# Optimization experiments

Measured on AMD Instinct MI355X. Metric: run time of the kernel, lower is better.

## Reference

```python
import jax, jax.numpy as jnp
import numpy as np

N_NODES = 100000
N_EDGES = 600000
VOCAB = 50000
EMBED_DIM = 128
HIDDEN_DIM = 128


def gcn_conv(h, W, b, src, dst, n_nodes):
    """PyG GCNConv: x' = D^{-1/2} (A+I) D^{-1/2} X W + b.
    src/dst already include self-loops."""
    hw = h @ W                                   # [N, out]
    deg = jnp.zeros((n_nodes,), hw.dtype).at[dst].add(1.0)   # in-degree incl. self-loop
    dinv = jax.lax.rsqrt(deg)                    # deg >= 1 thanks to self-loops
    norm = dinv[src] * dinv[dst]                 # [E+N]
    msgs = norm[:, None] * hw[src]               # gather [E+N, out]
    out = jnp.zeros_like(hw).at[dst].add(msgs)   # scatter-aggregate
    return out + b


def setup_inputs() -> dict:
    key = jax.random.key(0)
    ks = jax.random.split(key, 8)
    x = jax.random.randint(ks[0], (N_NODES,), 0, VOCAB, dtype=jnp.int64 if jax.config.jax_enable_x64 else jnp.int32)
    edge_index = jax.random.randint(ks[1], (2, N_EDGES), 0, N_NODES, dtype=jnp.int32)
    emb = jax.random.normal(ks[2], (VOCAB, EMBED_DIM), dtype=jnp.float32)
    # Glorot-style scale for GCN weights
    W1 = jax.random.normal(ks[3], (EMBED_DIM, HIDDEN_DIM), dtype=jnp.float32) * (1.0 / np.sqrt(EMBED_DIM))
    b1 = jnp.zeros((HIDDEN_DIM,), dtype=jnp.float32)
    W2 = jax.random.normal(ks[4], (HIDDEN_DIM, HIDDEN_DIM), dtype=jnp.float32) * (1.0 / np.sqrt(HIDDEN_DIM))
    b2 = jnp.zeros((HIDDEN_DIM,), dtype=jnp.float32)
    return {"x": x, "edge_index": edge_index, "emb": emb, "W1": W1, "b1": b1, "W2": W2, "b2": b2}


def reference(x, edge_index, emb, W1, b1, W2, b2):
    n = x.shape[0]
    loops = jnp.arange(n, dtype=edge_index.dtype)
    src = jnp.concatenate([edge_index[0], loops])  # add self-loops once
    dst = jnp.concatenate([edge_index[1], loops])
    h = emb[x]                                     # [N, embed_dim] embedding lookup
    h = jax.nn.relu(gcn_conv(h, W1, b1, src, dst, n))
    h = jax.nn.relu(gcn_conv(h, W2, b2, src, dst, n))
    return h
```

## Files before the change

### kernel.cpp

```cpp
#include <hip/hip_runtime.h>
#include <hip/hip_fp16.h>


#define NDIM 128
#define PAD_K 136
#define SCAN_IPT 4
#define SCAN_BLK 256
#define SCAN_IPB (SCAN_BLK * SCAN_IPT)

typedef __bf16 bf16x8 __attribute__((ext_vector_type(8)));
typedef float f32x4 __attribute__((ext_vector_type(4)));

__device__ __forceinline__ float bf2f(unsigned short u) {
    union { unsigned int i; float f; } c;
    c.i = (unsigned int)u << 16;
    return c.f;
}
__device__ __forceinline__ unsigned short f2bf(float f) {
    __bf16 b = (__bf16)f;
    return __builtin_bit_cast(unsigned short, b);
}
__device__ __forceinline__ unsigned short f2h(float f) {
    __half h = __float2half_rn(f);
    return __builtin_bit_cast(unsigned short, h);
}
__device__ __forceinline__ float h2f(unsigned short u) {
    return __half2float(__builtin_bit_cast(__half, u));
}
__device__ __forceinline__ void unpack8(uint4 q, float* f) {
    f[0] = bf2f((unsigned short)(q.x & 0xffff));
    f[1] = bf2f((unsigned short)(q.x >> 16));
    f[2] = bf2f((unsigned short)(q.y & 0xffff));
    f[3] = bf2f((unsigned short)(q.y >> 16));
    f[4] = bf2f((unsigned short)(q.z & 0xffff));
    f[5] = bf2f((unsigned short)(q.z >> 16));
    f[6] = bf2f((unsigned short)(q.w & 0xffff));
    f[7] = bf2f((unsigned short)(q.w >> 16));
}

__global__ void degree_count(const int* __restrict__ dst, int* __restrict__ cnt, int E) {
    const int stride = gridDim.x * blockDim.x;
    int e = blockIdx.x * blockDim.x + threadIdx.x;
#pragma unroll
    for (int k = 0; k < 2; ++k) {
        int ee = e + k * stride;
        if (ee < E) atomicAdd(&cnt[dst[ee]], 1);
    }
}

__global__ void scan_blocks(const int* __restrict__ in, int* __restrict__ out,
                            int* __restrict__ bsums, int n) {
    __shared__ int lds[SCAN_BLK];
    const int t = threadIdx.x;
    const int base = blockIdx.x * SCAN_IPB + t * SCAN_IPT;
    int v[SCAN_IPT];
    int s = 0;
#pragma unroll
    for (int k = 0; k < SCAN_IPT; ++k) { v[k] = (base + k < n) ? in[base + k] : 0; s += v[k]; }
    lds[t] = s;
    __syncthreads();
    for (int off = 1; off < SCAN_BLK; off <<= 1) {
        int x = (t >= off) ? lds[t - off] : 0;
        __syncthreads();
        lds[t] += x;
        __syncthreads();
    }
    if (t == SCAN_BLK - 1) bsums[blockIdx.x] = lds[t];
    int run = (t == 0) ? 0 : lds[t - 1];
#pragma unroll
    for (int k = 0; k < SCAN_IPT; ++k) {
        if (base + k < n) out[base + k] = run;
        run += v[k];
    }
}

__global__ void scan_partials(int* __restrict__ bsums, int nb) {
    __shared__ int lds[128];
    const int t = threadIdx.x;
    lds[t] = (t < nb) ? bsums[t] : 0;
    __syncthreads();
    for (int off = 1; off < 128; off <<= 1) {
        int x = (t >= off) ? lds[t - off] : 0;
        __syncthreads();
        lds[t] += x;
        __syncthreads();
    }
    if (t < nb) bsums[t] = (t == 0) ? 0 : lds[t - 1];
}

__global__ void add_offsets_dinv_wt(int* __restrict__ rp, const int* __restrict__ bsums,
                                    const int* __restrict__ cnt, float* __restrict__ dinv, int n,
                                    int nblkA,
                                    const float* __restrict__ W1, const float* __restrict__ W2,
                                    unsigned short* __restrict__ WT1,
                                    unsigned short* __restrict__ WT2) {
    if ((int)blockIdx.x < nblkA) {
        int i = blockIdx.x * blockDim.x + threadIdx.x;
        if (i < n) {
            rp[i] += bsums[i / SCAN_IPB];
            dinv[i] = rsqrtf((float)cnt[i] + 1.0f);
        }
    } else {
        int c = (blockIdx.x - nblkA) * blockDim.x + threadIdx.x;
        int cc = c & 16383;
        int j = cc >> 7, k = cc & 127;
        if (c < 16384) WT1[cc] = f2bf(W1[k * 128 + j]);
        else if (c < 32768) WT2[cc] = f2bf(W2[k * 128 + j]);
    }
}

__global__ __launch_bounds__(256, 4)
void gemm1_fill(const float* __restrict__ emb, const unsigned short* __restrict__ WT1,
                unsigned short* __restrict__ embW1, int V, int gemmBlocks,
                const int* __restrict__ src, const int* __restrict__ dst,
                int* __restrict__ rp, const int* __restrict__ x,
                const float* __restrict__ dinv, int2* __restrict__ ew, int E,
                int fillBlocks) {
    __shared__ __bf16 sBT[128 * PAD_K];
    const int tid = threadIdx.x;

    if ((int)blockIdx.x < gemmBlocks) {
        const int rbase = blockIdx.x * 64;
        {
            const uint4* bsrc = (const uint4*)WT1;
#pragma unroll
            for (int i = 0; i < 8; ++i) {
                int c = tid + i * 256;
                int j = c >> 4, u = c & 15;
                *(uint4*)&sBT[j * PAD_K + u * 8] = bsrc[c];
            }
        }
        __syncthreads();

        const int wave = tid >> 6, lane = tid & 63;
        const int quad = lane >> 4, lrow = lane & 15;
        int arow = rbase + wave * 16 + lrow;
        if (arow >= V) arow = V - 1;

        f32x4 acc[8];
#pragma unroll
        for (int nt = 0; nt < 8; ++nt) acc[nt] = (f32x4)0.0f;

#pragma unroll
        for (int ks = 0; ks < 4; ++ks) {
            const int kb = ks * 32 + quad * 8;
            const float4* A4 = (const float4*)emb;
            float4 v0 = A4[(size_t)arow * 32 + (kb >> 2)];
            float4 v1 = A4[(size_t)arow * 32 + (kb >> 2) + 1];
            bf16x8 a = (bf16x8){(__bf16)v0.x, (__bf16)v0.y, (__bf16)v0.z, (__bf16)v0.w,
                                (__bf16)v1.x, (__bf16)v1.y, (__bf16)v1.z, (__bf16)v1.w};
#pragma unroll
            for (int nt = 0; nt < 8; ++nt) {
                bf16x8 b = *(const bf16x8*)&sBT[(nt * 16 + lrow) * PAD_K + kb];
                acc[nt] = __builtin_amdgcn_mfma_f32_16x16x32_bf16(a, b, acc[nt], 0, 0, 0);
            }
        }

#pragma unroll
        for (int r = 0; r < 4; ++r) {
            int grow = rbase + wave * 16 + quad * 4 + r;
            if (grow < V) {
                unsigned short* orow = embW1 + (size_t)grow * NDIM + lrow;
#pragma unroll
                for (int nt = 0; nt < 8; ++nt)
                    orow[nt * 16] = f2bf(acc[nt][r]);
            }
        }
    } else {
        const int bid = blockIdx.x - gemmBlocks;
        const int stride = fillBlocks * 256;
        int e = bid * 256 + tid;
#pragma unroll
        for (int k = 0; k < 2; ++k, e += stride) {
            if (e < E) {
                int d = dst[e], s = src[e];
                int xs = x[s];
                float ds = dinv[s];
                int p = atomicAdd(&rp[d], 1);
                ew[p] = make_int2(s, (int)(((unsigned)f2h(ds) << 16) | (unsigned)xs));
            }
        }
    }
}

__global__ __launch_bounds__(256, 4)
void gemm_mfma_b(const unsigned short* __restrict__ Asrc, const unsigned short* __restrict__ WTb,
                 const float* __restrict__ dinv, unsigned short* __restrict__ outb, int n) {
    __shared__ __bf16 sBT[128 * PAD_K];
    const int tid = threadIdx.x;
    const int rbase = blockIdx.x * 64;

    {
        const uint4* bsrc = (const uint4*)WTb;
#pragma unroll
        for (int i = 0; i < 8; ++i) {
            int c = tid + i * 256;
            int j = c >> 4, u = c & 15;
            *(uint4*)&sBT[j * PAD_K + u * 8] = bsrc[c];
        }
    }
    __syncthreads();

    const int wave = tid >> 6, lane = tid & 63;
    const int quad = lane >> 4, lrow = lane & 15;
    int arow = rbase + wave * 16 + lrow;
    if (arow >= n) arow = n - 1;

    f32x4 acc[8];
#pragma unroll
    for (int nt = 0; nt < 8; ++nt) acc[nt] = (f32x4)0.0f;

#pragma unroll
    for (int ks = 0; ks < 4; ++ks) {
        const int kb = ks * 32 + quad * 8;
        bf16x8 a = *(const bf16x8*)(Asrc + (size_t)arow * 128 + kb);
#pragma unroll
        for (int nt = 0; nt < 8; ++nt) {
            bf16x8 b = *(const bf16x8*)&sBT[(nt * 16 + lrow) * PAD_K + kb];
            acc[nt] = __builtin_amdgcn_mfma_f32_16x16x32_bf16(a, b, acc[nt], 0, 0, 0);
        }
    }

#pragma unroll
    for (int r = 0; r < 4; ++r) {
        int grow = rbase + wave * 16 + quad * 4 + r;
        if (grow < n) {
            float dsc = dinv[grow];
            unsigned short* orow = outb + (size_t)grow * NDIM + lrow;
#pragma unroll
            for (int nt = 0; nt < 8; ++nt)
                orow[nt * 16] = f2bf(dsc * acc[nt][r]);
        }
    }
}

__global__ void aggregate1(const unsigned short* __restrict__ tab, const int* __restrict__ x,
                           const int* __restrict__ rp, const int2* __restrict__ ew,
                           const float* __restrict__ dinv, const float* __restrict__ bias,
                           unsigned short* __restrict__ outb, int n, int half) {
    int t = blockIdx.x * blockDim.x + threadIdx.x;
    int g = t >> 4, u = t & 15;
    if (g >= half) return;
    const uint4* tab4 = (const uint4*)tab;
    const int i0 = g, i1 = g + half;
    const bool has1 = (i1 < n);
    float di0 = dinv[i0];
    float di1 = has1 ? dinv[i1] : 0.0f;
    float acc0[8], acc1[8];
    {
        float f[8];
        unpack8(tab4[(size_t)x[i0] * 16 + u], f);
#pragma unroll
        for (int k = 0; k < 8; ++k) acc0[k] = di0 * f[k];
    }
    if (has1) {
        float f[8];
        unpack8(tab4[(size_t)x[i1] * 16 + u], f);
#pragma unroll
        for (int k = 0; k < 8; ++k) acc1[k] = di1 * f[k];
    }
    int j0 = (i0 == 0) ? 0 : rp[i0 - 1];
    const int e0 = rp[i0];
    int j1 = has1 ? rp[i1 - 1] : 0;
    const int e1 = has1 ? rp[i1] : 0;

    while (j0 + 2 <= e0 && j1 + 2 <= e1) {
        int2 a0 = ew[j0], a1 = ew[j0 + 1], c0 = ew[j1], c1 = ew[j1 + 1];
        uint4 qa0 = tab4[(size_t)(a0.y & 0xffff) * 16 + u];
        uint4 qa1 = tab4[(size_t)(a1.y & 0xffff) * 16 + u];
        uint4 qc0 = tab4[(size_t)(c0.y & 0xffff) * 16 + u];
        uint4 qc1 = tab4[(size_t)(c1.y & 0xffff) * 16 + u];
        float fa0[8], fa1[8], fc0[8], fc1[8];
        unpack8(qa0, fa0); unpack8(qa1, fa1); unpack8(qc0, fc0); unpack8(qc1, fc1);
        float na0 = h2f((unsigned short)((unsigned)a0.y >> 16));
        float na1 = h2f((unsigned short)((unsigned)a1.y >> 16));
        float nc0 = h2f((unsigned short)((unsigned)c0.y >> 16));
        float nc1 = h2f((unsigned short)((unsigned)c1.y >> 16));
#pragma unroll
        for (int k = 0; k < 8; ++k) {
            acc0[k] += fmaf(na0, fa0[k], na1 * fa1[k]);
            acc1[k] += fmaf(nc0, fc0[k], nc1 * fc1[k]);
        }
        j0 += 2; j1 += 2;
    }
    for (; j0 + 2 <= e0; j0 += 2) {
        int2 a0 = ew[j0], a1 = ew[j0 + 1];
        uint4 qa0 = tab4[(size_t)(a0.y & 0xffff) * 16 + u];
        uint4 qa1 = tab4[(size_t)(a1.y & 0xffff) * 16 + u];
        float fa0[8], fa1[8];
        unpack8(qa0, fa0); unpack8(qa1, fa1);
        float na0 = h2f((unsigned short)((unsigned)a0.y >> 16));
        float na1 = h2f((unsigned short)((unsigned)a1.y >> 16));
#pragma unroll
        for (int k = 0; k < 8; ++k) acc0[k] += fmaf(na0, fa0[k], na1 * fa1[k]);
    }
    if (j0 < e0) {
        int2 a = ew[j0];
        uint4 q = tab4[(size_t)(a.y & 0xffff) * 16 + u];
        float f[8];
        unpack8(q, f);
        float nm = h2f((unsigned short)((unsigned)a.y >> 16));
#pragma unroll
        for (int k = 0; k < 8; ++k) acc0[k] = fmaf(nm, f[k], acc0[k]);
    }
    for (; j1 + 2 <= e1; j1 += 2) {
        int2 c0 = ew[j1], c1 = ew[j1 + 1];
        uint4 qc0 = tab4[(size_t)(c0.y & 0xffff) * 16 + u];
        uint4 qc1 = tab4[(size_t)(c1.y & 0xffff) * 16 + u];
        float fc0[8], fc1[8];
        unpack8(qc0, fc0); unpack8(qc1, fc1);
        float nc0 = h2f((unsigned short)((unsigned)c0.y >> 16));
        float nc1 = h2f((unsigned short)((unsigned)c1.y >> 16));
#pragma unroll
        for (int k = 0; k < 8; ++k) acc1[k] += fmaf(nc0, fc0[k], nc1 * fc1[k]);
    }
    if (j1 < e1) {
        int2 c = ew[j1];
        uint4 q = tab4[(size_t)(c.y & 0xffff) * 16 + u];
        float f[8];
        unpack8(q, f);
        float nm = h2f((unsigned short)((unsigned)c.y >> 16));
#pragma unroll
        for (int k = 0; k < 8; ++k) acc1[k] = fmaf(nm, f[k], acc1[k]);
    }

    const float4 b0 = ((const float4*)bias)[u * 2];
    const float4 b1 = ((const float4*)bias)[u * 2 + 1];
    {
        float r[8];
        r[0] = fmaxf(fmaf(di0, acc0[0], b0.x), 0.0f);
        r[1] = fmaxf(fmaf(di0, acc0[1], b0.y), 0.0f);
        r[2] = fmaxf(fmaf(di0, acc0[2], b0.z), 0.0f);
        r[3] = fmaxf(fmaf(di0, acc0[3], b0.w), 0.0f);
        r[4] = fmaxf(fmaf(di0, acc0[4], b1.x), 0.0f);
        r[5] = fmaxf(fmaf(di0, acc0[5], b1.y), 0.0f);
        r[6] = fmaxf(fmaf(di0, acc0[6], b1.z), 0.0f);
        r[7] = fmaxf(fmaf(di0, acc0[7], b1.w), 0.0f);
        uint4 o;
        o.x = (unsigned)f2bf(r[0]) | ((unsigned)f2bf(r[1]) << 16);
        o.y = (unsigned)f2bf(r[2]) | ((unsigned)f2bf(r[3]) << 16);
        o.z = (unsigned)f2bf(r[4]) | ((unsigned)f2bf(r[5]) << 16);
        o.w = (unsigned)f2bf(r[6]) | ((unsigned)f2bf(r[7]) << 16);
        ((uint4*)outb)[(size_t)i0 * 16 + u] = o;
    }
    if (has1) {
        float r[8];
        r[0] = fmaxf(fmaf(di1, acc1[0], b0.x), 0.0f);
        r[1] = fmaxf(fmaf(di1, acc1[1], b0.y), 0.0f);
        r[2] = fmaxf(fmaf(di1, acc1[2], b0.z), 0.0f);
        r[3] = fmaxf(fmaf(di1, acc1[3], b0.w), 0.0f);
        r[4] = fmaxf(fmaf(di1, acc1[4], b1.x), 0.0f);
        r[5] = fmaxf(fmaf(di1, acc1[5], b1.y), 0.0f);
        r[6] = fmaxf(fmaf(di1, acc1[6], b1.z), 0.0f);
        r[7] = fmaxf(fmaf(di1, acc1[7], b1.w), 0.0f);
        uint4 o;
        o.x = (unsigned)f2bf(r[0]) | ((unsigned)f2bf(r[1]) << 16);
        o.y = (unsigned)f2bf(r[2]) | ((unsigned)f2bf(r[3]) << 16);
        o.z = (unsigned)f2bf(r[4]) | ((unsigned)f2bf(r[5]) << 16);
        o.w = (unsigned)f2bf(r[6]) | ((unsigned)f2bf(r[7]) << 16);
        ((uint4*)outb)[(size_t)i1 * 16 + u] = o;
    }
}

__global__ void aggregate2(const unsigned short* __restrict__ vs, const int* __restrict__ rp,
                           const int2* __restrict__ ew, const float* __restrict__ dinv,
                           const float* __restrict__ bias, float* __restrict__ out,
                           int n, int half) {
    int t = blockIdx.x * blockDim.x + threadIdx.x;
    int g = t >> 4, u = t & 15;
    if (g >= half) return;
    const uint4* vs4 = (const uint4*)vs;
    const int i0 = g, i1 = g + half;
    const bool has1 = (i1 < n);
    float acc0[8], acc1[8];
    unpack8(vs4[(size_t)i0 * 16 + u], acc0);
    if (has1) unpack8(vs4[(size_t)i1 * 16 + u], acc1);
    int j0 = (i0 == 0) ? 0 : rp[i0 - 1];
    const int e0 = rp[i0];
    int j1 = has1 ? rp[i1 - 1] : 0;
    const int e1 = has1 ? rp[i1] : 0;

    while (j0 + 2 <= e0 && j1 + 2 <= e1) {
        int s00 = ew[j0].x, s01 = ew[j0 + 1].x, s10 = ew[j1].x, s11 = ew[j1 + 1].x;
        uint4 q00 = vs4[(size_t)s00 * 16 + u];
        uint4 q01 = vs4[(size_t)s01 * 16 + u];
        uint4 q10 = vs4[(size_t)s10 * 16 + u];
        uint4 q11 = vs4[(size_t)s11 * 16 + u];
        float f00[8], f01[8], f10[8], f11[8];
        unpack8(q00, f00); unpack8(q01, f01); unpack8(q10, f10); unpack8(q11, f11);
#pragma unroll
        for (int k = 0; k < 8; ++k) {
            acc0[k] += f00[k] + f01[k];
            acc1[k] += f10[k] + f11[k];
        }
        j0 += 2; j1 += 2;
    }
    for (; j0 + 2 <= e0; j0 += 2) {
        int s00 = ew[j0].x, s01 = ew[j0 + 1].x;
        uint4 q00 = vs4[(size_t)s00 * 16 + u];
        uint4 q01 = vs4[(size_t)s01 * 16 + u];
        float f00[8], f01[8];
        unpack8(q00, f00); unpack8(q01, f01);
#pragma unroll
        for (int k = 0; k < 8; ++k) acc0[k] += f00[k] + f01[k];
    }
    if (j0 < e0) {
        uint4 q = vs4[(size_t)ew[j0].x * 16 + u];
        float f[8];
        unpack8(q, f);
#pragma unroll
        for (int k = 0; k < 8; ++k) acc0[k] += f[k];
    }
    for (; j1 + 2 <= e1; j1 += 2) {
        int s10 = ew[j1].x, s11 = ew[j1 + 1].x;
        uint4 q10 = vs4[(size_t)s10 * 16 + u];
        uint4 q11 = vs4[(size_t)s11 * 16 + u];
        float f10[8], f11[8];
        unpack8(q10, f10); unpack8(q11, f11);
#pragma unroll
        for (int k = 0; k < 8; ++k) acc1[k] += f10[k] + f11[k];
    }
    if (j1 < e1) {
        uint4 q = vs4[(size_t)ew[j1].x * 16 + u];
        float f[8];
        unpack8(q, f);
#pragma unroll
        for (int k = 0; k < 8; ++k) acc1[k] += f[k];
    }

    const float4 b0 = ((const float4*)bias)[u * 2];
    const float4 b1 = ((const float4*)bias)[u * 2 + 1];
    {
        float di = dinv[i0];
        float4 r0, r1;
        r0.x = fmaxf(fmaf(di, acc0[0], b0.x), 0.0f);
        r0.y = fmaxf(fmaf(di, acc0[1], b0.y), 0.0f);
        r0.z = fmaxf(fmaf(di, acc0[2], b0.z), 0.0f);
        r0.w = fmaxf(fmaf(di, acc0[3], b0.w), 0.0f);
        r1.x = fmaxf(fmaf(di, acc0[4], b1.x), 0.0f);
        r1.y = fmaxf(fmaf(di, acc0[5], b1.y), 0.0f);
        r1.z = fmaxf(fmaf(di, acc0[6], b1.z), 0.0f);
        r1.w = fmaxf(fmaf(di, acc0[7], b1.w), 0.0f);
        ((float4*)out)[(size_t)i0 * 32 + u * 2] = r0;
        ((float4*)out)[(size_t)i0 * 32 + u * 2 + 1] = r1;
    }
    if (has1) {
        float di = dinv[i1];
        float4 r0, r1;
        r0.x = fmaxf(fmaf(di, acc1[0], b0.x), 0.0f);
        r0.y = fmaxf(fmaf(di, acc1[1], b0.y), 0.0f);
        r0.z = fmaxf(fmaf(di, acc1[2], b0.z), 0.0f);
        r0.w = fmaxf(fmaf(di, acc1[3], b0.w), 0.0f);
        r1.x = fmaxf(fmaf(di, acc1[4], b1.x), 0.0f);
        r1.y = fmaxf(fmaf(di, acc1[5], b1.y), 0.0f);
        r1.z = fmaxf(fmaf(di, acc1[6], b1.z), 0.0f);
        r1.w = fmaxf(fmaf(di, acc1[7], b1.w), 0.0f);
        ((float4*)out)[(size_t)i1 * 32 + u * 2] = r0;
        ((float4*)out)[(size_t)i1 * 32 + u * 2 + 1] = r1;
    }
}

extern "C" void kernel_launch(void* const* d_in, const int* in_sizes, int n_in,
                              void* d_out, int out_size, void* d_ws, size_t ws_size,
                              hipStream_t stream) {
    const int* x = (const int*)d_in[0];
    const int* edge_index = (const int*)d_in[1];
    const float* emb = (const float*)d_in[2];
    const float* W1 = (const float*)d_in[3];
    const float* b1 = (const float*)d_in[4];
    const float* W2 = (const float*)d_in[5];
    const float* b2 = (const float*)d_in[6];
    float* out = (float*)d_out;

    const int N = in_sizes[0];
    const int E = in_sizes[1] / 2;
    const int V = in_sizes[2] / NDIM;
    const int* src = edge_index;
    const int* dst = edge_index + E;

    char* p = (char*)d_ws;
    auto alloc = [&](size_t bytes) {
        char* q = p;
        p += (bytes + 511) & ~(size_t)511;
        return q;
    };
    int* cnt = (int*)alloc((size_t)N * sizeof(int));
    int* rp = (int*)alloc((size_t)N * sizeof(int));
    float* dinv = (float*)alloc((size_t)N * sizeof(float));
    int* bsums = (int*)alloc(128 * sizeof(int));
    int2* ew = (int2*)alloc((size_t)E * sizeof(int2));
    unsigned short* WT1 = (unsigned short*)alloc(16384 * sizeof(unsigned short));
    unsigned short* WT2 = (unsigned short*)alloc(16384 * sizeof(unsigned short));
    unsigned short* embW1 = (unsigned short*)alloc((size_t)V * NDIM * sizeof(unsigned short));
    unsigned short* h1b = (unsigned short*)alloc((size_t)N * NDIM * sizeof(unsigned short));
    unsigned short* vs2 = (unsigned short*)alloc((size_t)N * NDIM * sizeof(unsigned short));
    (void)ws_size;

    const int NB = (N + SCAN_IPB - 1) / SCAN_IPB;
    const int nblkA = (N + 255) / 256;
    const int half = (N + 1) / 2;
    const int gemmBlocks = (V + 63) / 64;
    const int fillBlocks = (E / 2 + 255) / 256;

    hipMemsetAsync(cnt, 0, (size_t)N * sizeof(int), stream);
    degree_count<<<(E / 2 + 255) / 256, 256, 0, stream>>>(dst, cnt, E);
    scan_blocks<<<NB, SCAN_BLK, 0, stream>>>(cnt, rp, bsums, N);
    scan_partials<<<1, 128, 0, stream>>>(bsums, NB);
    add_offsets_dinv_wt<<<nblkA + 128, 256, 0, stream>>>(rp, bsums, cnt, dinv, N, nblkA,
                                                         W1, W2, WT1, WT2);

    gemm1_fill<<<gemmBlocks + fillBlocks, 256, 0, stream>>>(
        emb, WT1, embW1, V, gemmBlocks, src, dst, rp, x, dinv, ew, E, fillBlocks);

    const int agg_blocks = (int)(((size_t)half * 16 + 255) / 256);

    aggregate1<<<agg_blocks, 256, 0, stream>>>(embW1, x, rp, ew, dinv, b1, h1b, N, half);
    gemm_mfma_b<<<(N + 63) / 64, 256, 0, stream>>>(h1b, WT2, dinv, vs2, N);
    aggregate2<<<agg_blocks, 256, 0, stream>>>(vs2, rp, ew, dinv, b2, out, N, half);
}
```

Measured before the change: 242.1 us.

## Restructure CSR build: single-block scan fused into GEMM1, separate edge fill

Replaces the multi-kernel degree count, block scan, partial scan and offset-add sequence with three launches. The first counts degrees and transposes the weights. The second has block 0 scan the degree counts serially while the other blocks run the embedding GEMM. The third fills the edge list. This cuts kernel launches and grid-wide dependencies, and hides the scan behind the GEMM work. The cost is that the scan now runs in a single block over about 100k entries in roughly 98 sequential chunks, which may become the critical path. The edge fill also no longer overlaps with the GEMM.

```diff
diff --git a/kernel.cpp b/kernel.cpp
--- a/kernel.cpp
+++ b/kernel.cpp
@@ -4,9 +4,6 @@
 
 #define NDIM 128
 #define PAD_K 136
-#define SCAN_IPT 4
-#define SCAN_BLK 256
-#define SCAN_IPB (SCAN_BLK * SCAN_IPT)
 
 typedef __bf16 bf16x8 __attribute__((ext_vector_type(8)));
 typedef float f32x4 __attribute__((ext_vector_type(4)));
@@ -38,149 +35,121 @@
     f[7] = bf2f((unsigned short)(q.w >> 16));
 }
 
-__global__ void degree_count(const int* __restrict__ dst, int* __restrict__ cnt, int E) {
-    const int stride = gridDim.x * blockDim.x;
-    int e = blockIdx.x * blockDim.x + threadIdx.x;
-#pragma unroll
-    for (int k = 0; k < 2; ++k) {
-        int ee = e + k * stride;
-        if (ee < E) atomicAdd(&cnt[dst[ee]], 1);
-    }
-}
-
-__global__ void scan_blocks(const int* __restrict__ in, int* __restrict__ out,
-                            int* __restrict__ bsums, int n) {
-    __shared__ int lds[SCAN_BLK];
-    const int t = threadIdx.x;
-    const int base = blockIdx.x * SCAN_IPB + t * SCAN_IPT;
-    int v[SCAN_IPT];
-    int s = 0;
-#pragma unroll
-    for (int k = 0; k < SCAN_IPT; ++k) { v[k] = (base + k < n) ? in[base + k] : 0; s += v[k]; }
-    lds[t] = s;
-    __syncthreads();
-    for (int off = 1; off < SCAN_BLK; off <<= 1) {
-        int x = (t >= off) ? lds[t - off] : 0;
-        __syncthreads();
-        lds[t] += x;
-        __syncthreads();
-    }
-    if (t == SCAN_BLK - 1) bsums[blockIdx.x] = lds[t];
-    int run = (t == 0) ? 0 : lds[t - 1];
-#pragma unroll
-    for (int k = 0; k < SCAN_IPT; ++k) {
-        if (base + k < n) out[base + k] = run;
-        run += v[k];
-    }
-}
-
-__global__ void scan_partials(int* __restrict__ bsums, int nb) {
-    __shared__ int lds[128];
-    const int t = threadIdx.x;
-    lds[t] = (t < nb) ? bsums[t] : 0;
-    __syncthreads();
-    for (int off = 1; off < 128; off <<= 1) {
-        int x = (t >= off) ? lds[t - off] : 0;
-        __syncthreads();
-        lds[t] += x;
-        __syncthreads();
-    }
-    if (t < nb) bsums[t] = (t == 0) ? 0 : lds[t - 1];
-}
-
-__global__ void add_offsets_dinv_wt(int* __restrict__ rp, const int* __restrict__ bsums,
-                                    const int* __restrict__ cnt, float* __restrict__ dinv, int n,
-                                    int nblkA,
-                                    const float* __restrict__ W1, const float* __restrict__ W2,
-                                    unsigned short* __restrict__ WT1,
-                                    unsigned short* __restrict__ WT2) {
-    if ((int)blockIdx.x < nblkA) {
-        int i = blockIdx.x * blockDim.x + threadIdx.x;
-        if (i < n) {
-            rp[i] += bsums[i / SCAN_IPB];
-            dinv[i] = rsqrtf((float)cnt[i] + 1.0f);
-        }
-    } else {
-        int c = (blockIdx.x - nblkA) * blockDim.x + threadIdx.x;
+__global__ void count_wt(const int* __restrict__ dst, int* __restrict__ cnt, int E, int nWT,
+                         const float* __restrict__ W1, const float* __restrict__ W2,
+                         unsigned short* __restrict__ WT1, unsigned short* __restrict__ WT2) {
+    if ((int)blockIdx.x < nWT) {
+        int c = blockIdx.x * blockDim.x + threadIdx.x;
         int cc = c & 16383;
         int j = cc >> 7, k = cc & 127;
         if (c < 16384) WT1[cc] = f2bf(W1[k * 128 + j]);
         else if (c < 32768) WT2[cc] = f2bf(W2[k * 128 + j]);
+    } else {
+        int e = (blockIdx.x - nWT) * blockDim.x + threadIdx.x;
+        if (e < E) atomicAdd(&cnt[dst[e]], 1);
     }
 }
 
 __global__ __launch_bounds__(256, 4)
-void gemm1_fill(const float* __restrict__ emb, const unsigned short* __restrict__ WT1,
-                unsigned short* __restrict__ embW1, int V, int gemmBlocks,
-                const int* __restrict__ src, const int* __restrict__ dst,
-                int* __restrict__ rp, const int* __restrict__ x,
-                const float* __restrict__ dinv, int2* __restrict__ ew, int E,
-                int fillBlocks) {
+void scan_gemm1(const int* __restrict__ cnt, int* __restrict__ rp, float* __restrict__ dinv,
+                int n, const float* __restrict__ emb, const unsigned short* __restrict__ WT1,
+                unsigned short* __restrict__ embW1, int V) {
     __shared__ __bf16 sBT[128 * PAD_K];
     const int tid = threadIdx.x;
 
-    if ((int)blockIdx.x < gemmBlocks) {
-        const int rbase = blockIdx.x * 64;
-        {
-            const uint4* bsrc = (const uint4*)WT1;
-#pragma unroll
-            for (int i = 0; i < 8; ++i) {
-                int c = tid + i * 256;
-                int j = c >> 4, u = c & 15;
-                *(uint4*)&sBT[j * PAD_K + u * 8] = bsrc[c];
+    if (blockIdx.x == 0) {
+        int* lds = (int*)sBT;
+        int carry = 0;
+        for (int base = 0; base < n; base += 1024) {
+            const int idx = base + tid * 4;
+            int v[4];
+            int s = 0;
+#pragma unroll
+            for (int k = 0; k < 4; ++k) {
+                v[k] = (idx + k < n) ? cnt[idx + k] : 0;
+                s += v[k];
             }
-        }
-        __syncthreads();
-
-        const int wave = tid >> 6, lane = tid & 63;
-        const int quad = lane >> 4, lrow = lane & 15;
-        int arow = rbase + wave * 16 + lrow;
-        if (arow >= V) arow = V - 1;
-
-        f32x4 acc[8];
-#pragma unroll
-        for (int nt = 0; nt < 8; ++nt) acc[nt] = (f32x4)0.0f;
-
-#pragma unroll
-        for (int ks = 0; ks < 4; ++ks) {
-            const int kb = ks * 32 + quad * 8;
-            const float4* A4 = (const float4*)emb;
-            float4 v0 = A4[(size_t)arow * 32 + (kb >> 2)];
-            float4 v1 = A4[(size_t)arow * 32 + (kb >> 2) + 1];
-            bf16x8 a = (bf16x8){(__bf16)v0.x, (__bf16)v0.y, (__bf16)v0.z, (__bf16)v0.w,
-                                (__bf16)v1.x, (__bf16)v1.y, (__bf16)v1.z, (__bf16)v1.w};
-#pragma unroll
-            for (int nt = 0; nt < 8; ++nt) {
-                bf16x8 b = *(const bf16x8*)&sBT[(nt * 16 + lrow) * PAD_K + kb];
-                acc[nt] = __builtin_amdgcn_mfma_f32_16x16x32_bf16(a, b, acc[nt], 0, 0, 0);
+#pragma unroll
+            for (int k = 0; k < 4; ++k)
+                if (idx + k < n) dinv[idx + k] = rsqrtf((float)v[k] + 1.0f);
+            lds[tid] = s;
+            __syncthreads();
+            for (int off = 1; off < 256; off <<= 1) {
+                int x = (tid >= off) ? lds[tid - off] : 0;
+                __syncthreads();
+                lds[tid] += x;
+                __syncthreads();
             }
-        }
-
-#pragma unroll
-        for (int r = 0; r < 4; ++r) {
-            int grow = rbase + wave * 16 + quad * 4 + r;
-            if (grow < V) {
-                unsigned short* orow = embW1 + (size_t)grow * NDIM + lrow;
-#pragma unroll
-                for (int nt = 0; nt < 8; ++nt)
-                    orow[nt * 16] = f2bf(acc[nt][r]);
+            int run = carry + ((tid == 0) ? 0 : lds[tid - 1]);
+#pragma unroll
+            for (int k = 0; k < 4; ++k) {
+                if (idx + k < n) rp[idx + k] = run;
+                run += v[k];
             }
-        }
-    } else {
-        const int bid = blockIdx.x - gemmBlocks;
-        const int stride = fillBlocks * 256;
-        int e = bid * 256 + tid;
-#pragma unroll
-        for (int k = 0; k < 2; ++k, e += stride) {
-            if (e < E) {
-                int d = dst[e], s = src[e];
-                int xs = x[s];
-                float ds = dinv[s];
-                int p = atomicAdd(&rp[d], 1);
-                ew[p] = make_int2(s, (int)(((unsigned)f2h(ds) << 16) | (unsigned)xs));
-            }
-        }
-    }
+            carry += lds[255];
+            __syncthreads();
+        }
+        return;
+    }
+
+    const int rbase = (blockIdx.x - 1) * 64;
+    {
+        const uint4* bsrc = (const uint4*)WT1;
+#pragma unroll
+        for (int i = 0; i < 8; ++i) {
+            int c = tid + i * 256;
+            int j = c >> 4, u = c & 15;
+            *(uint4*)&sBT[j * PAD_K + u * 8] = bsrc[c];
+        }
+    }
+    __syncthreads();
+
+    const int wave = tid >> 6, lane = tid & 63;
+    const int quad = lane >> 4, lrow = lane & 15;
+    int arow = rbase + wave * 16 + lrow;
+    if (arow >= V) arow = V - 1;
+
+    f32x4 acc[8];
+#pragma unroll
+    for (int nt = 0; nt < 8; ++nt) acc[nt] = (f32x4)0.0f;
+
+#pragma unroll
+    for (int ks = 0; ks < 4; ++ks) {
+        const int kb = ks * 32 + quad * 8;
+        const float4* A4 = (const float4*)emb;
+        float4 v0 = A4[(size_t)arow * 32 + (kb >> 2)];
+        float4 v1 = A4[(size_t)arow * 32 + (kb >> 2) + 1];
+        bf16x8 a = (bf16x8){(__bf16)v0.x, (__bf16)v0.y, (__bf16)v0.z, (__bf16)v0.w,
+                            (__bf16)v1.x, (__bf16)v1.y, (__bf16)v1.z, (__bf16)v1.w};
+#pragma unroll
+        for (int nt = 0; nt < 8; ++nt) {
+            bf16x8 b = *(const bf16x8*)&sBT[(nt * 16 + lrow) * PAD_K + kb];
+            acc[nt] = __builtin_amdgcn_mfma_f32_16x16x32_bf16(a, b, acc[nt], 0, 0, 0);
+        }
+    }
+
+#pragma unroll
+    for (int r = 0; r < 4; ++r) {
+        int grow = rbase + wave * 16 + quad * 4 + r;
+        if (grow < V) {
+            unsigned short* orow = embW1 + (size_t)grow * NDIM + lrow;
+#pragma unroll
+            for (int nt = 0; nt < 8; ++nt)
+                orow[nt * 16] = f2bf(acc[nt][r]);
+        }
+    }
+}
+
+__global__ void fill_edges(const int* __restrict__ src, const int* __restrict__ dst,
+                           int* __restrict__ rp, const int* __restrict__ x,
+                           const float* __restrict__ dinv, int2* __restrict__ ew, int E) {
+    int e = blockIdx.x * blockDim.x + threadIdx.x;
+    if (e >= E) return;
+    int d = dst[e], s = src[e];
+    int xs = x[s];
+    float ds = dinv[s];
+    int p = atomicAdd(&rp[d], 1);
+    ew[p] = make_int2(s, (int)(((unsigned)f2h(ds) << 16) | (unsigned)xs));
 }
 
 __global__ __launch_bounds__(256, 4)
@@ -487,7 +456,6 @@
     int* cnt = (int*)alloc((size_t)N * sizeof(int));
     int* rp = (int*)alloc((size_t)N * sizeof(int));
     float* dinv = (float*)alloc((size_t)N * sizeof(float));
-    int* bsums = (int*)alloc(128 * sizeof(int));
     int2* ew = (int2*)alloc((size_t)E * sizeof(int2));
     unsigned short* WT1 = (unsigned short*)alloc(16384 * sizeof(unsigned short));
     unsigned short* WT2 = (unsigned short*)alloc(16384 * sizeof(unsigned short));
@@ -496,21 +464,15 @@
     unsigned short* vs2 = (unsigned short*)alloc((size_t)N * NDIM * sizeof(unsigned short));
     (void)ws_size;
 
-    const int NB = (N + SCAN_IPB - 1) / SCAN_IPB;
-    const int nblkA = (N + 255) / 256;
     const int half = (N + 1) / 2;
-    const int gemmBlocks = (V + 63) / 64;
-    const int fillBlocks = (E / 2 + 255) / 256;
+    const int nWT = 128;
+    const int cntBlocks = (E + 255) / 256;
+    const int gemm1Blocks = (V + 63) / 64;
 
     hipMemsetAsync(cnt, 0, (size_t)N * sizeof(int), stream);
-    degree_count<<<(E / 2 + 255) / 256, 256, 0, stream>>>(dst, cnt, E);
-    scan_blocks<<<NB, SCAN_BLK, 0, stream>>>(cnt, rp, bsums, N);
-    scan_partials<<<1, 128, 0, stream>>>(bsums, NB);
-    add_offsets_dinv_wt<<<nblkA + 128, 256, 0, stream>>>(rp, bsums, cnt, dinv, N, nblkA,
-                                                         W1, W2, WT1, WT2);
-
-    gemm1_fill<<<gemmBlocks + fillBlocks, 256, 0, stream>>>(
-        emb, WT1, embW1, V, gemmBlocks, src, dst, rp, x, dinv, ew, E, fillBlocks);
+    count_wt<<<nWT + cntBlocks, 256, 0, stream>>>(dst, cnt, E, nWT, W1, W2, WT1, WT2);
+    scan_gemm1<<<1 + gemm1Blocks, 256, 0, stream>>>(cnt, rp, dinv, N, emb, WT1, embW1, V);
+    fill_edges<<<(E + 255) / 256, 256, 0, stream>>>(src, dst, rp, x, dinv, ew, E);
 
     const int agg_blocks = (int)(((size_t)half * 16 + 255) / 256);
 
```

Result: slower. 434.4 us (+79.4%).
